# Optimization experiments

Hardware: AMD Instinct MI355X
Metric: run time of the kernel (lower is better)

Reference implementation:

```python
import jax, jax.numpy as jnp
import numpy as np
import math

EPS = 1e-5  # torch LayerNorm default
B, T, H, W, C = 2, 16, 32, 32, 768
NH = 12
HD = C // NH


def layernorm(x, w, b):
    mu = jnp.mean(x, axis=-1, keepdims=True)
    var = jnp.var(x, axis=-1, keepdims=True)
    return (x - mu) * jax.lax.rsqrt(var + EPS) * w + b


def setup_inputs() -> dict:
    key = jax.random.key(0)
    ks = jax.random.split(key, 4)
    s = 1.0 / math.sqrt(C)
    return {
        "x": jax.random.normal(ks[0], (B, T, H, W, C), dtype=jnp.float32),
        "ln1_w": jnp.ones((C,), jnp.float32),
        "ln1_b": jnp.zeros((C,), jnp.float32),
        "Wqkv": jax.random.normal(ks[1], (3 * C, C), jnp.float32) * s,
        "bqkv": jnp.zeros((3 * C,), jnp.float32),
        "ln2_w": jnp.ones((C,), jnp.float32),
        "ln2_b": jnp.zeros((C,), jnp.float32),
        "Wout": jax.random.normal(ks[2], (C, C), jnp.float32) * s,
        "bout": jnp.zeros((C,), jnp.float32),
    }


def reference(x, ln1_w, ln1_b, Wqkv, bqkv, ln2_w, ln2_b, Wout, bout):
    b, t, h, w, c = x.shape
    inp = x
    y = layernorm(x, ln1_w, ln1_b)
    qkv = jnp.einsum('bthwc,fc->bthwf', y, Wqkv) + bqkv          # (B,T,H,W,3C)
    qkv = qkv.reshape(b, t, h, w, NH, 3 * HD)
    q, k, v = jnp.split(qkv, 3, axis=-1)                          # each (B,T,H,W,NH,HD)
    scale = 1.0 / math.sqrt(HD)
    # attention over the time axis, batched over (b,h,w,heads)
    scores = jnp.einsum('bthwnd,bshwnd->bhwnts', q, k) * scale    # (B,H,W,NH,T,T)
    attn = jax.nn.softmax(scores, axis=-1)
    o = jnp.einsum('bhwnts,bshwnd->bthwnd', attn, v)              # (B,T,H,W,NH,HD)
    o = o.reshape(b, t, h, w, c)
    o = layernorm(o, ln2_w, ln2_b)
    o = jnp.einsum('bthwc,fc->bthwf', o, Wout) + bout
    return o + inp
```

## Files before the change

kernel.cpp:

```cpp
#include <hip/hip_runtime.h>

typedef unsigned short u16;
typedef __attribute__((ext_vector_type(8))) short frag8;
typedef __attribute__((ext_vector_type(4))) float f32x4;

static constexpr int C = 768;
static constexpr int F3 = 2304;
static constexpr int MROWS = 32768;
static constexpr float LNEPS = 1e-5f;

__device__ __forceinline__ float bfu2f(u16 u){
  union { unsigned u; float f; } x; x.u = (unsigned)u << 16; return x.f;
}
__device__ __forceinline__ u16 f2bfu(float f){
  union { float f; unsigned u; } x; x.f = f;
  unsigned r = x.u + 0x7fffu + ((x.u >> 16) & 1u);
  return (u16)(r >> 16);
}

__device__ __forceinline__ void gload16(const void* g, void* l){
  __builtin_amdgcn_global_load_lds(
      (const __attribute__((address_space(1))) void*)g,
      (__attribute__((address_space(3))) void*)l, 16, 0, 0);
}

__global__ __launch_bounds__(256) void cvt_bf16(const float* __restrict__ src,
                                                u16* __restrict__ dst, int n){
  int i = blockIdx.x * 256 + threadIdx.x;
  if (i < n) dst[i] = f2bfu(src[i]);
}

__global__ __launch_bounds__(256) void ln1_kernel(const float* __restrict__ x,
    const float* __restrict__ w, const float* __restrict__ b, u16* __restrict__ y){
  const int lane = threadIdx.x & 63, wid = threadIdx.x >> 6;
  const size_t row = (size_t)blockIdx.x * 4 + wid;
  const float4* xr = reinterpret_cast<const float4*>(x + row * C);
  float v[12];
  #pragma unroll
  for (int j = 0; j < 3; j++){
    float4 t = xr[lane + j*64];
    v[j*4+0]=t.x; v[j*4+1]=t.y; v[j*4+2]=t.z; v[j*4+3]=t.w;
  }
  float s = 0.f, ss = 0.f;
  #pragma unroll
  for (int j = 0; j < 12; j++){ s += v[j]; ss += v[j]*v[j]; }
  #pragma unroll
  for (int o = 32; o; o >>= 1){ s += __shfl_xor(s, o, 64); ss += __shfl_xor(ss, o, 64); }
  const float mu = s * (1.f/768.f);
  const float rs = rsqrtf(ss*(1.f/768.f) - mu*mu + LNEPS);
  ushort4* yr = reinterpret_cast<ushort4*>(y + row * C);
  const float4* wv = reinterpret_cast<const float4*>(w);
  const float4* bv = reinterpret_cast<const float4*>(b);
  #pragma unroll
  for (int j = 0; j < 3; j++){
    float4 wj = wv[lane + j*64], bj = bv[lane + j*64];
    ushort4 o4;
    o4.x = f2bfu((v[j*4+0]-mu)*rs*wj.x + bj.x);
    o4.y = f2bfu((v[j*4+1]-mu)*rs*wj.y + bj.y);
    o4.z = f2bfu((v[j*4+2]-mu)*rs*wj.z + bj.z);
    o4.w = f2bfu((v[j*4+3]-mu)*rs*wj.w + bj.w);
    yr[lane + j*64] = o4;
  }
}

template<int MODE>
__global__ __launch_bounds__(512, 2) void gemm_bt(
    const u16* __restrict__ A, const u16* __restrict__ Bw,
    const float* __restrict__ bias, const float* __restrict__ resid,
    void* __restrict__ Cout, int Ndim, int K)
{
  __shared__ __align__(16) char lds[131072];
  const int tid = threadIdx.x;
  const int lane = tid & 63, wid = tid >> 6;
  const int wm = wid >> 2, wn = wid & 3;
  const int ntn = Ndim >> 8;
  const int cpx = (int)gridDim.x >> 3;
  const int wg = ((int)blockIdx.x & 7) * cpx + ((int)blockIdx.x >> 3);
  const int bm = wg / ntn, bn = wg % ntn;
  const int m0 = bm << 8, n0 = bn << 8;

  const int rp = lane >> 2;
  const int rr = rp ^ ((rp >> 2) & 1);
  const int qq = (lane & 3) ^ (rr & 3);
  const u16* aS = A  + (size_t)(m0 + wid*16 + rr) * K + qq*8;
  const u16* bS = Bw + (size_t)(n0 + wid*16 + rr) * K + qq*8;
  const size_t half128 = 128 * (size_t)K;

  const int fr = lane & 15, kq = lane >> 4;
  const int sig16 = (((fr ^ ((fr >> 2) & 1)) << 2) | (kq ^ (fr & 3))) * 16;

  f32x4 acc[8][4] = {};

  auto stA = [&](int ts){
    char* lb = lds + (ts & 3)*32768;
    gload16(aS + ts*32,           lb + wid*1024);
    gload16(aS + ts*32 + half128, lb + (8+wid)*1024);
  };
  auto stB = [&](int ts){
    char* lb = lds + (ts & 3)*32768 + 16384;
    gload16(bS + ts*32,           lb + wid*1024);
    gload16(bS + ts*32 + half128, lb + (8+wid)*1024);
  };

  stA(0); stB(0); stA(1); stB(1); stA(2);
  asm volatile("s_waitcnt vmcnt(6)" ::: "memory");
  __builtin_amdgcn_s_barrier();

  for (int t = 0; t < 24; ++t){
    const char* base = lds + (t & 3)*32768;
    int tb = t + 2; if (tb >= 24) tb -= 24;
    int ta = t + 3; if (ta >= 24) ta -= 24;
    frag8 af[4], bf[4], ag[4];

    #pragma unroll
    for (int mf = 0; mf < 4; mf++)
      af[mf] = *reinterpret_cast<const frag8*>(base + (wm*8+mf)*1024 + sig16);
    #pragma unroll
    for (int nf = 0; nf < 4; nf++)
      bf[nf] = *reinterpret_cast<const frag8*>(base + 16384 + (wn*4+nf)*1024 + sig16);
    stB(tb);
    asm volatile("s_waitcnt vmcnt(6)" ::: "memory");
    asm volatile("s_waitcnt lgkmcnt(0)" ::: "memory");
    __builtin_amdgcn_sched_barrier(0);
    __builtin_amdgcn_s_barrier();
    __builtin_amdgcn_s_setprio(1);
    #pragma unroll
    for (int mf = 0; mf < 4; mf++)
      #pragma unroll
      for (int nf = 0; nf < 4; nf++)
        acc[mf][nf] = __builtin_amdgcn_mfma_f32_16x16x32_bf16(bf[nf], af[mf], acc[mf][nf], 0, 0, 0);
    __builtin_amdgcn_s_setprio(0);

    #pragma unroll
    for (int mf = 0; mf < 4; mf++)
      ag[mf] = *reinterpret_cast<const frag8*>(base + (wm*8+4+mf)*1024 + sig16);
    stA(ta);
    asm volatile("s_waitcnt vmcnt(6)" ::: "memory");
    asm volatile("s_waitcnt lgkmcnt(0)" ::: "memory");
    __builtin_amdgcn_sched_barrier(0);
    __builtin_amdgcn_s_barrier();
    __builtin_amdgcn_s_setprio(1);
    #pragma unroll
    for (int mf = 0; mf < 4; mf++)
      #pragma unroll
      for (int nf = 0; nf < 4; nf++)
        acc[4+mf][nf] = __builtin_amdgcn_mfma_f32_16x16x32_bf16(bf[nf], ag[mf], acc[4+mf][nf], 0, 0, 0);
    __builtin_amdgcn_s_setprio(0);
  }
  asm volatile("s_waitcnt vmcnt(0)" ::: "memory");

  const int em = fr, en = kq * 4;
  float4 bb[4];
  #pragma unroll
  for (int nf = 0; nf < 4; nf++)
    bb[nf] = *reinterpret_cast<const float4*>(bias + n0 + wn*64 + nf*16 + en);

  #pragma unroll
  for (int mf = 0; mf < 8; mf++){
    const size_t m = (size_t)(m0 + wm*128 + mf*16 + em);
    #pragma unroll
    for (int nf = 0; nf < 4; nf++){
      const int n = n0 + wn*64 + nf*16 + en;
      if (MODE == 0){
        ushort4 o4;
        o4.x = f2bfu(acc[mf][nf][0] + bb[nf].x);
        o4.y = f2bfu(acc[mf][nf][1] + bb[nf].y);
        o4.z = f2bfu(acc[mf][nf][2] + bb[nf].z);
        o4.w = f2bfu(acc[mf][nf][3] + bb[nf].w);
        *reinterpret_cast<ushort4*>((u16*)Cout + m * Ndim + n) = o4;
      } else {
        const float4 rr4 = *reinterpret_cast<const float4*>(resid + m * Ndim + n);
        float4 o4;
        o4.x = acc[mf][nf][0] + bb[nf].x + rr4.x;
        o4.y = acc[mf][nf][1] + bb[nf].y + rr4.y;
        o4.z = acc[mf][nf][2] + bb[nf].z + rr4.z;
        o4.w = acc[mf][nf][3] + bb[nf].w + rr4.w;
        *reinterpret_cast<float4*>((float*)Cout + m * Ndim + n) = o4;
      }
    }
  }
}

__global__ __launch_bounds__(256) void attn_ln2(const u16* __restrict__ qkv,
    const float* __restrict__ w2, const float* __restrict__ b2, u16* __restrict__ y2){
  __shared__ __align__(16) u16 S[16][2312];
  __shared__ float SP[4][16][17];
  const int tid = threadIdx.x;
  const int lane = tid & 63, wid = tid >> 6;
  const int bid = blockIdx.x;
  const int w = bid & 31, h = (bid >> 5) & 31, b = bid >> 10;
  const size_t rbase = (size_t)b*16384 + h*32 + w;

  #pragma unroll
  for (int it = 0; it < 18; it++){
    const int e = tid + it*256;
    const int t = e / 288, c = e % 288;
    const uint4 v = *reinterpret_cast<const uint4*>(qkv + (rbase + (size_t)t*1024)*F3 + c*8);
    *reinterpret_cast<uint4*>(&S[t][c*8]) = v;
  }
  __syncthreads();

  const int g = lane >> 4, sj = lane & 15;
  #pragma unroll
  for (int hh = 0; hh < 3; hh++){
    const int n = wid*3 + hh;
    const int q0 = n*192, k0 = q0 + 64, v0 = q0 + 128;
    float accv[4] = {0.f, 0.f, 0.f, 0.f};
    #pragma unroll
    for (int dc = 0; dc < 8; dc++){
      union { uint4 u; u16 s[8]; } kc;
      kc.u = *reinterpret_cast<const uint4*>(&S[sj][k0 + dc*8]);
      #pragma unroll
      for (int i = 0; i < 4; i++){
        union { uint4 u; u16 s[8]; } qc;
        qc.u = *reinterpret_cast<const uint4*>(&S[g + 4*i][q0 + dc*8]);
        #pragma unroll
        for (int e = 0; e < 8; e++)
          accv[i] += bfu2f(qc.s[e]) * bfu2f(kc.s[e]);
      }
    }
    #pragma unroll
    for (int i = 0; i < 4; i++){
      float sc = accv[i] * 0.125f;
      float mx = sc;
      #pragma unroll
      for (int o = 1; o < 16; o <<= 1) mx = fmaxf(mx, __shfl_xor(mx, o, 16));
      float p = __expf(sc - mx);
      float sm = p;
      #pragma unroll
      for (int o = 1; o < 16; o <<= 1) sm += __shfl_xor(sm, o, 16);
      SP[wid][g + 4*i][sj] = p / sm;
    }
    float ot[16];
    #pragma unroll
    for (int t = 0; t < 16; t++){
      float o = 0.f;
      #pragma unroll
      for (int s = 0; s < 16; s++) o += SP[wid][t][s] * bfu2f(S[s][v0 + lane]);
      ot[t] = o;
    }
    #pragma unroll
    for (int t = 0; t < 16; t++) S[t][v0 + lane] = f2bfu(ot[t]);
  }
  __syncthreads();

  #pragma unroll
  for (int rq = 0; rq < 4; rq++){
    const int t = wid*4 + rq;
    float v[12];
    #pragma unroll
    for (int j = 0; j < 12; j++) v[j] = bfu2f(S[t][j*192 + 128 + lane]);
    float s = 0.f, ss = 0.f;
    #pragma unroll
    for (int j = 0; j < 12; j++){ s += v[j]; ss += v[j]*v[j]; }
    #pragma unroll
    for (int o = 32; o; o >>= 1){ s += __shfl_xor(s, o, 64); ss += __shfl_xor(ss, o, 64); }
    const float mu = s * (1.f/768.f);
    const float rs = rsqrtf(ss*(1.f/768.f) - mu*mu + LNEPS);
    u16* yr = y2 + (rbase + (size_t)t*1024) * C;
    #pragma unroll
    for (int j = 0; j < 12; j++){
      const int c = j*64 + lane;
      yr[c] = f2bfu((v[j]-mu)*rs*w2[c] + b2[c]);
    }
  }
}

extern "C" void kernel_launch(void* const* d_in, const int* in_sizes, int n_in,
                              void* d_out, int out_size, void* d_ws, size_t ws_size,
                              hipStream_t stream){
  const float* x    = (const float*)d_in[0];
  const float* ln1w = (const float*)d_in[1];
  const float* ln1b = (const float*)d_in[2];
  const float* Wqkv = (const float*)d_in[3];
  const float* bqkv = (const float*)d_in[4];
  const float* ln2w = (const float*)d_in[5];
  const float* ln2b = (const float*)d_in[6];
  const float* Wout = (const float*)d_in[7];
  const float* bout = (const float*)d_in[8];
  float* out = (float*)d_out;

  char* ws = (char*)d_ws;
  u16* qkv = (u16*)ws;
  u16* y   = (u16*)(ws + 150994944);
  u16* wq  = (u16*)(ws + 201326592);
  u16* wo  = (u16*)(ws + 204865536);

  cvt_bf16<<<(F3*C + 255)/256, 256, 0, stream>>>(Wqkv, wq, F3*C);
  cvt_bf16<<<(C*C + 255)/256, 256, 0, stream>>>(Wout, wo, C*C);
  ln1_kernel<<<MROWS/4, 256, 0, stream>>>(x, ln1w, ln1b, y);
  gemm_bt<0><<<(MROWS/256)*(F3/256), 512, 0, stream>>>(y, wq, bqkv, nullptr, qkv, F3, C);
  attn_ln2<<<2*32*32, 256, 0, stream>>>(qkv, ln2w, ln2b, y);
  gemm_bt<1><<<(MROWS/256)*(C/256), 512, 0, stream>>>(y, wo, bout, x, out, C, C);
}
```

Before: 356.7 us.

## Shrink GEMM tile to 128x256 with double-buffered LDS for higher occupancy

Changes the bf16 GEMM block tile from 256x256 to 128x256. The four-stage LDS pipeline becomes a two-stage one, LDS usage drops from 128KB to 48KB, and the launch bound is raised to 4 blocks per CU. Each wave now holds half as many accumulators and runs one MFMA phase per k-step, with a single prefetch stage and two barriers per iteration. The aim is more resident waves and a larger grid to hide latency, at the cost of less operand reuse per tile and shallower prefetching.

```diff
diff --git a/kernel.cpp b/kernel.cpp
--- a/kernel.cpp
+++ b/kernel.cpp
@@ -64,12 +64,12 @@
 }
 
 template<int MODE>
-__global__ __launch_bounds__(512, 2) void gemm_bt(
+__global__ __launch_bounds__(512, 4) void gemm_bt(
     const u16* __restrict__ A, const u16* __restrict__ Bw,
     const float* __restrict__ bias, const float* __restrict__ resid,
     void* __restrict__ Cout, int Ndim, int K)
 {
-  __shared__ __align__(16) char lds[131072];
+  __shared__ __align__(16) char lds[49152];
   const int tid = threadIdx.x;
   const int lane = tid & 63, wid = tid >> 6;
   const int wm = wid >> 2, wn = wid & 3;
@@ -77,7 +77,7 @@
   const int cpx = (int)gridDim.x >> 3;
   const int wg = ((int)blockIdx.x & 7) * cpx + ((int)blockIdx.x >> 3);
   const int bm = wg / ntn, bn = wg % ntn;
-  const int m0 = bm << 8, n0 = bn << 8;
+  const int m0 = bm << 7, n0 = bn << 8;
 
   const int rp = lane >> 2;
   const int rr = rp ^ ((rp >> 2) & 1);
@@ -89,40 +89,33 @@
   const int fr = lane & 15, kq = lane >> 4;
   const int sig16 = (((fr ^ ((fr >> 2) & 1)) << 2) | (kq ^ (fr & 3))) * 16;
 
-  f32x4 acc[8][4] = {};
-
-  auto stA = [&](int ts){
-    char* lb = lds + (ts & 3)*32768;
+  f32x4 acc[4][4] = {};
+
+  auto stage = [&](int ts){
+    char* lb = lds + (ts & 1)*24576;
     gload16(aS + ts*32,           lb + wid*1024);
-    gload16(aS + ts*32 + half128, lb + (8+wid)*1024);
+    gload16(bS + ts*32,           lb + 8192 + wid*1024);
+    gload16(bS + ts*32 + half128, lb + 8192 + (8+wid)*1024);
   };
-  auto stB = [&](int ts){
-    char* lb = lds + (ts & 3)*32768 + 16384;
-    gload16(bS + ts*32,           lb + wid*1024);
-    gload16(bS + ts*32 + half128, lb + (8+wid)*1024);
-  };
-
-  stA(0); stB(0); stA(1); stB(1); stA(2);
-  asm volatile("s_waitcnt vmcnt(6)" ::: "memory");
-  __builtin_amdgcn_s_barrier();
+
+  stage(0);
 
   for (int t = 0; t < 24; ++t){
-    const char* base = lds + (t & 3)*32768;
-    int tb = t + 2; if (tb >= 24) tb -= 24;
-    int ta = t + 3; if (ta >= 24) ta -= 24;
-    frag8 af[4], bf[4], ag[4];
-
-    #pragma unroll
-    for (int mf = 0; mf < 4; mf++)
-      af[mf] = *reinterpret_cast<const frag8*>(base + (wm*8+mf)*1024 + sig16);
-    #pragma unroll
-    for (int nf = 0; nf < 4; nf++)
-      bf[nf] = *reinterpret_cast<const frag8*>(base + 16384 + (wn*4+nf)*1024 + sig16);
-    stB(tb);
-    asm volatile("s_waitcnt vmcnt(6)" ::: "memory");
+    int tn = t + 1; if (tn >= 24) tn = 0;
+    stage(tn);
+    asm volatile("s_waitcnt vmcnt(3)" ::: "memory");
+    __builtin_amdgcn_s_barrier();
+
+    const char* base = lds + (t & 1)*24576;
+    const char* pa = base + (wm*4)*1024 + sig16;
+    const char* pb = base + 8192 + (wn*4)*1024 + sig16;
+    frag8 af[4], bf[4];
+    #pragma unroll
+    for (int mf = 0; mf < 4; mf++) af[mf] = *reinterpret_cast<const frag8*>(pa + mf*1024);
+    #pragma unroll
+    for (int nf = 0; nf < 4; nf++) bf[nf] = *reinterpret_cast<const frag8*>(pb + nf*1024);
     asm volatile("s_waitcnt lgkmcnt(0)" ::: "memory");
     __builtin_amdgcn_sched_barrier(0);
-    __builtin_amdgcn_s_barrier();
     __builtin_amdgcn_s_setprio(1);
     #pragma unroll
     for (int mf = 0; mf < 4; mf++)
@@ -130,22 +123,7 @@
       for (int nf = 0; nf < 4; nf++)
         acc[mf][nf] = __builtin_amdgcn_mfma_f32_16x16x32_bf16(bf[nf], af[mf], acc[mf][nf], 0, 0, 0);
     __builtin_amdgcn_s_setprio(0);
-
-    #pragma unroll
-    for (int mf = 0; mf < 4; mf++)
-      ag[mf] = *reinterpret_cast<const frag8*>(base + (wm*8+4+mf)*1024 + sig16);
-    stA(ta);
-    asm volatile("s_waitcnt vmcnt(6)" ::: "memory");
-    asm volatile("s_waitcnt lgkmcnt(0)" ::: "memory");
-    __builtin_amdgcn_sched_barrier(0);
     __builtin_amdgcn_s_barrier();
-    __builtin_amdgcn_s_setprio(1);
-    #pragma unroll
-    for (int mf = 0; mf < 4; mf++)
-      #pragma unroll
-      for (int nf = 0; nf < 4; nf++)
-        acc[4+mf][nf] = __builtin_amdgcn_mfma_f32_16x16x32_bf16(bf[nf], ag[mf], acc[4+mf][nf], 0, 0, 0);
-    __builtin_amdgcn_s_setprio(0);
   }
   asm volatile("s_waitcnt vmcnt(0)" ::: "memory");
 
@@ -156,8 +134,8 @@
     bb[nf] = *reinterpret_cast<const float4*>(bias + n0 + wn*64 + nf*16 + en);
 
   #pragma unroll
-  for (int mf = 0; mf < 8; mf++){
-    const size_t m = (size_t)(m0 + wm*128 + mf*16 + em);
+  for (int mf = 0; mf < 4; mf++){
+    const size_t m = (size_t)(m0 + wm*64 + mf*16 + em);
     #pragma unroll
     for (int nf = 0; nf < 4; nf++){
       const int n = n0 + wn*64 + nf*16 + en;
@@ -289,7 +267,7 @@
   cvt_bf16<<<(F3*C + 255)/256, 256, 0, stream>>>(Wqkv, wq, F3*C);
   cvt_bf16<<<(C*C + 255)/256, 256, 0, stream>>>(Wout, wo, C*C);
   ln1_kernel<<<MROWS/4, 256, 0, stream>>>(x, ln1w, ln1b, y);
-  gemm_bt<0><<<(MROWS/256)*(F3/256), 512, 0, stream>>>(y, wq, bqkv, nullptr, qkv, F3, C);
+  gemm_bt<0><<<(MROWS/128)*(F3/256), 512, 0, stream>>>(y, wq, bqkv, nullptr, qkv, F3, C);
   attn_ln2<<<2*32*32, 256, 0, stream>>>(qkv, ln2w, ln2b, y);
-  gemm_bt<1><<<(MROWS/256)*(C/256), 512, 0, stream>>>(y, wo, bout, x, out, C, C);
-}
+  gemm_bt<1><<<(MROWS/128)*(C/256), 512, 0, stream>>>(y, wo, bout, x, out, C, C);
+}
```

Measured after the change: 345.5 us. 1.03x faster.
